# Performance work log

Hardware: AMD Instinct MI355X
Metric: run time of the kernel (lower is better)

The kernel has to match this reference:

```python
import jax, jax.numpy as jnp
import numpy as np

N_NODES, N_EDGES, B, K = 10000, 100000, 8192, 10
MEM = EMB = TE = EF = 172
HID = 80
MSG = 2 * MEM + TE + EF  # 688


def setup_inputs() -> dict:
    key = jax.random.key(0)
    ks = jax.random.split(key, 24)
    f = jax.random.normal
    inp = {
        'timestamps': jax.random.uniform(ks[0], (B,)) * 100.0,
        'edge_features': f(ks[1], (N_EDGES, EF)),
        'temporal_node_features': f(ks[2], (N_NODES, MEM)),
        'node_mem': 0.1 * f(ks[3], (N_NODES, MEM)),
        'last_updated': jax.random.uniform(ks[4], (N_NODES,)) * 50.0,
        'nbr_edge_times': jax.random.uniform(ks[5], (B, K)) * 100.0,
        # TimeEncode params (fixed init from source)
        'time_w': jnp.asarray(1.0 / 10 ** np.linspace(0, 9, TE), jnp.float32),
        'time_b': jnp.zeros((TE,), jnp.float32),
        # RNNCell params
        'rnn_Wih': 0.05 * f(ks[6], (MEM, MSG)),
        'rnn_Whh': 0.05 * f(ks[7], (MEM, MEM)),
        'rnn_bih': jnp.zeros((MEM,)),
        'rnn_bhh': jnp.zeros((MEM,)),
        # layer linears (n_layers=1)
        'lin1_w': 0.05 * f(ks[8], (EMB, EMB + TE + EF)),
        'lin1_b': jnp.zeros((EMB,)),
        'lin2_w': 0.05 * f(ks[9], (EMB, MEM + TE + EMB)),
        'lin2_b': jnp.zeros((EMB,)),
        # MLP head
        'mlp_w1': 0.05 * f(ks[10], (HID, EMB)),
        'mlp_b1': jnp.zeros((HID,)),
        'mlp_w2': 0.05 * f(ks[11], (10, HID)),
        'mlp_b2': jnp.zeros((10,)),
        'mlp_w3': 0.05 * f(ks[12], (1, 10)),
        'mlp_b3': jnp.zeros((1,)),
        'sources': jax.random.randint(ks[13], (B,), 0, N_NODES),
        'destinations': jax.random.randint(ks[14], (B,), 0, N_NODES),
        'edge_idxs': jax.random.randint(ks[15], (B,), 0, N_EDGES),
        'neighbors': jax.random.randint(ks[16], (B, K), 0, N_NODES),
        'nbr_edge_idxs': jax.random.randint(ks[17], (B, K), 0, N_EDGES),
    }
    return inp


def _time_enc(dt, w, b):
    # cos(Linear(1->D)(t)) from TimeEncode
    return jnp.cos(dt[..., None] * w + b)


def reference(timestamps, edge_features, temporal_node_features, node_mem,
              last_updated, nbr_edge_times, time_w, time_b,
              rnn_Wih, rnn_Whh, rnn_bih, rnn_bhh,
              lin1_w, lin1_b, lin2_w, lin2_b,
              mlp_w1, mlp_b1, mlp_w2, mlp_b2, mlp_w3, mlp_b3,
              sources, destinations, edge_idxs, neighbors, nbr_edge_idxs):
    # ---- get_message: gather memories + edge features + time-delta encoding
    ef = edge_features[edge_idxs]                         # [B, EF]
    src_mem = node_mem[sources]                           # [B, MEM]
    dst_mem = node_mem[destinations]                      # [B, MEM]
    dt = timestamps - last_updated[sources]               # [B]
    msg = jnp.concatenate([src_mem, dst_mem, ef, _time_enc(dt, time_w, time_b)], axis=1)  # [B, MSG]

    # ---- message aggregation: keep LAST message per unique source node
    n = node_mem.shape[0]
    b = sources.shape[0]
    last_idx = jnp.full((n,), -1, jnp.int32).at[sources].max(jnp.arange(b, dtype=jnp.int32))
    upd = last_idx >= 0                                   # [N] nodes receiving a message
    gi = jnp.clip(last_idx, 0)
    node_msg = msg[gi]                                    # [N, MSG]

    # ---- RNNCell memory update (masked to updated nodes)
    h_new = jnp.tanh(node_msg @ rnn_Wih.T + rnn_bih + node_mem @ rnn_Whh.T + rnn_bhh)
    mem = jnp.where(upd[:, None], h_new, node_mem)        # [N, MEM]

    # ---- compute_embedding, n_layers = 1 (layer-0 feats = mem + temporal feats)
    src_feat = mem[sources] + temporal_node_features[sources]      # [B, MEM]
    nbr_feat = mem[neighbors] + temporal_node_features[neighbors]  # [B, K, MEM]
    edge_t_enc = _time_enc(timestamps[:, None] - nbr_edge_times, time_w, time_b)  # [B, K, TE]
    nbr_ef = edge_features[nbr_edge_idxs]                           # [B, K, EF]
    nf = jnp.concatenate([nbr_feat, edge_t_enc, nbr_ef], axis=2)    # [B, K, MEM+TE+EF]
    h1 = jnp.einsum('bkf,ef->bke', nf, lin1_w) + lin1_b             # linear_1
    nbr_sum = jax.nn.relu(jnp.sum(h1, axis=1))                      # sum-aggregate, [B, EMB]
    src_t_enc = _time_enc(jnp.zeros_like(timestamps), time_w, time_b)  # cos(b), [B, TE]
    emb = jnp.concatenate([nbr_sum, src_feat, src_t_enc], axis=1) @ lin2_w.T + lin2_b  # [B, EMB]

    # ---- MLP head (dropout disabled / eval mode) + sigmoid
    h = jax.nn.relu(emb @ mlp_w1.T + mlp_b1)
    h = jax.nn.relu(h @ mlp_w2.T + mlp_b2)
    return jax.nn.sigmoid((h @ mlp_w3.T + mlp_b3)[:, 0])  # [B]
```

## Files before the change

### kernel.cpp

```cpp
#include <hip/hip_runtime.h>
#include <math.h>

#define N_NODES 10000
#define BB 8192
#define KK 10
#define D 172
#define HIDD 80

typedef _Float16 f16;
typedef f16 f16x8 __attribute__((ext_vector_type(8)));
typedef f16 f16x4 __attribute__((ext_vector_type(4)));
typedef float f32x4 __attribute__((ext_vector_type(4)));


__global__ void scatter_last(const int* __restrict__ sources, int* __restrict__ last_idx) {
    int b = blockIdx.x * blockDim.x + threadIdx.x;
    if (b < BB) atomicMax(&last_idx[sources[b]], b);
}

__global__ void compact_nodes(const int* __restrict__ last_idx, int* __restrict__ nid,
                              int* __restrict__ li_arr, int* __restrict__ cnt) {
    int n = blockIdx.x * blockDim.x + threadIdx.x;
    if (n < N_NODES) {
        int li = last_idx[n];
        if (li >= 0) { int p = atomicAdd(cnt, 1); nid[p] = n; li_arr[p] = li; }
    }
}

#define CR0 135168
#define CR1 (CR0 + 104448)
#define CR2 (CR1 + 67584)
#define CR3 (CR2 + 15360)
#define CR4 (CR3 + 192)
#define CR5 (CR4 + 220000)
#define CR6 (CR5 + 10001)

__global__ __launch_bounds__(256) void conv_weights(
    const float* __restrict__ Wih, const float* __restrict__ Whh,
    const float* __restrict__ lin1_w, const float* __restrict__ lin2_w,
    const float* __restrict__ w1,
    const float* __restrict__ bih, const float* __restrict__ bhh,
    const float* __restrict__ lin2_b, const float* __restrict__ tb,
    const float* __restrict__ node_mem, const float* __restrict__ tnf,
    f16* __restrict__ Wc, f16* __restrict__ W1, f16* __restrict__ W2,
    f16* __restrict__ Wm1, float* __restrict__ bcomb, float* __restrict__ embc,
    f16* __restrict__ FEAT, int* __restrict__ last_idx, int* __restrict__ cnt)
{
    const int idx = blockIdx.x * 256 + threadIdx.x;
    if (idx < CR0) {
        int n = idx / 704, k = idx % 704, seg = k / 176, kk = k % 176;
        float v = 0.f;
        if (n < D && kk < D) {
            v = Wih[n * 688 + seg * D + kk];
            if (seg == 0) v += Whh[n * D + kk];
        }
        Wc[idx] = (f16)v;
    } else if (idx < CR1) {
        int i = idx - CR0;
        int n = i / 544, k = i % 544, seg = k / 176, kk = k % 176;
        float v = 0.f;
        if (n < D && seg < 3 && kk < D) v = lin1_w[n * 516 + seg * D + kk];
        W1[i] = (f16)v;
    } else if (idx < CR2) {
        int i = idx - CR1;
        int n = i / 352, k = i % 352, seg = k / 176, kk = k % 176;
        float v = 0.f;
        if (n < D && kk < D) v = lin2_w[n * 516 + seg * D + kk];
        W2[i] = (f16)v;
    } else if (idx < CR3) {
        int i = idx - CR2;
        int n = i / 192, k = i % 192;
        Wm1[i] = (f16)((k < D) ? w1[n * D + k] : 0.f);
    } else if (idx < CR4) {
        int i = idx - CR3;
        if (i < D) {
            bcomb[i] = bih[i] + bhh[i];
            float acc = lin2_b[i];
            for (int j = 0; j < D; ++j) acc += lin2_w[i * 516 + 344 + j] * __cosf(tb[j]);
            embc[i] = acc;
        }
    } else if (idx < CR5) {
        int i = idx - CR4;
        int n = i / 22, k0 = (i % 22) * 8;
        f16x8 o;
        #pragma unroll
        for (int j = 0; j < 8; ++j) {
            int kk = k0 + j;
            float v = (kk < D) ? node_mem[(size_t)n * D + kk] + tnf[(size_t)n * D + kk] : 0.f;
            o[j] = (f16)v;
        }
        *(f16x8*)(FEAT + (size_t)n * 176 + k0) = o;
    } else if (idx < CR6) {
        int i = idx - CR5;
        if (i < N_NODES) last_idx[i] = -1;
        else *cnt = 0;
    }
}

#define LDA_R 712

__global__ __launch_bounds__(768) void gemm_rnn_fused(
    const f16* __restrict__ Wc, const float* __restrict__ bcomb,
    const int* __restrict__ nid, const int* __restrict__ li_arr, const int* __restrict__ cnt,
    const int* __restrict__ destinations, const int* __restrict__ edge_idxs,
    const float* __restrict__ timestamps, const float* __restrict__ last_updated,
    const float* __restrict__ node_mem, const float* __restrict__ edge_features,
    const float* __restrict__ tw, const float* __restrict__ tb,
    const float* __restrict__ tnf, f16* __restrict__ FEAT)
{
    const int c = *cnt;
    const int R0 = blockIdx.x * 16;
    if (R0 >= c) return;
    __shared__ f16 As[16 * LDA_R];
    __shared__ int s_n[16], s_dst[16], s_ei[16];
    __shared__ float s_dt[16];
    const int t = threadIdx.x;
    if (t < 16) {
        int i = R0 + t; if (i > c - 1) i = c - 1;
        int n = nid[i], li = li_arr[i];
        s_n[t] = n; s_dst[t] = destinations[li]; s_ei[t] = edge_idxs[li];
        s_dt[t] = timestamps[li] - last_updated[n];
    }
    __syncthreads();
    for (int idx = t; idx < 16 * 88; idx += 768) {
        int row = idx / 88, sub = idx - row * 88;
        int seg = sub / 22, cpos = sub - seg * 22, k0 = cpos * 8;
        f16x8 o;
        if (seg < 3) {
            int n = (seg == 0) ? s_n[row] : (seg == 1) ? s_dst[row] : s_ei[row];
            const float* src = ((seg < 2) ? node_mem : edge_features) + (size_t)n * D + k0;
            float4 lo = *(const float4*)src;
            float4 hi = (cpos < 21) ? *(const float4*)(src + 4) : make_float4(0.f, 0.f, 0.f, 0.f);
            o[0] = (f16)lo.x; o[1] = (f16)lo.y; o[2] = (f16)lo.z; o[3] = (f16)lo.w;
            o[4] = (f16)hi.x; o[5] = (f16)hi.y; o[6] = (f16)hi.z; o[7] = (f16)hi.w;
        } else {
            float dt = s_dt[row];
            #pragma unroll
            for (int j = 0; j < 8; ++j) {
                int kk = k0 + j;
                o[j] = (f16)((kk < D) ? __cosf(dt * tw[kk] + tb[kk]) : 0.f);
            }
        }
        *(f16x8*)(As + row * LDA_R + seg * 176 + k0) = o;
    }
    __syncthreads();
    const int w = t >> 6, l = t & 63;
    if (w >= 11) return;
    const int lane16 = l & 15, koff = (l >> 4) * 8;
    const int C0 = w * 16;
    const f16* Al = As + lane16 * LDA_R + koff;
    const f16* Bp = Wc + (size_t)(C0 + lane16) * 704 + koff;
    f32x4 acc = {};
    #pragma unroll 2
    for (int s = 0; s < 22; ++s) {
        f16x8 a = *(const f16x8*)(Al + s * 32);
        f16x8 b = *(const f16x8*)(Bp + s * 32);
        acc = __builtin_amdgcn_mfma_f32_16x16x32_f16(a, b, acc, 0, 0, 0);
    }
    const int col = C0 + lane16;
    const int rloc = (l >> 4) * 4;
    if (col < D) {
        const float bc = bcomb[col];
        #pragma unroll
        for (int reg = 0; reg < 4; ++reg) {
            int rl = rloc + reg;
            int r = R0 + rl;
            if (r >= c) continue;
            int n = s_n[rl];
            FEAT[(size_t)n * 176 + col] = (f16)(tanhf(acc[reg] + bc) + tnf[(size_t)n * D + col]);
        }
    }
}

#define LDA_1 552
#define LDA_2 360
#define LDE  200

__global__ __launch_bounds__(768) void embed_fused(
    const f16* __restrict__ W1, const float* __restrict__ lin1_b,
    const f16* __restrict__ W2, const float* __restrict__ embc,
    const f16* __restrict__ Wm1, const float* __restrict__ b1,
    const float* __restrict__ w2, const float* __restrict__ b2,
    const float* __restrict__ w3, const float* __restrict__ b3,
    const f16* __restrict__ FEAT, const float* __restrict__ edge_features,
    const float* __restrict__ timestamps, const float* __restrict__ nbr_edge_times,
    const int* __restrict__ neighbors, const int* __restrict__ nbr_edge_idxs,
    const int* __restrict__ sources,
    const float* __restrict__ tw, const float* __restrict__ tb,
    float* __restrict__ out)
{
    __shared__ f16 As[16 * LDA_1];
    __shared__ f16 Acat[16 * LDA_2];
    __shared__ float sH[16][84];
    __shared__ float s_w2[10 * HIDD];
    __shared__ float s_b2[10], s_w3[10], s_b3;
    __shared__ int s_nbr[160], s_nei[160], s_src[16];
    __shared__ float s_net[160], s_ts[16];
    const int t = threadIdx.x;
    const int R0 = blockIdx.x * 16;
    for (int i = t; i < 10 * HIDD; i += 768) s_w2[i] = w2[i];
    if (t < 10) { s_b2[t] = b2[t]; s_w3[t] = w3[t]; }
    if (t == 10) s_b3 = b3[0];
    if (t >= 64 && t < 224) {
        int u = t - 64;
        s_nbr[u] = neighbors[R0 * KK + u];
    } else if (t >= 224 && t < 384) {
        int u = t - 224;
        s_nei[u] = nbr_edge_idxs[R0 * KK + u];
        s_net[u] = nbr_edge_times[R0 * KK + u];
    } else if (t >= 384 && t < 400) {
        s_ts[t - 384] = timestamps[R0 + t - 384];
    } else if (t >= 400 && t < 416) {
        s_src[t - 400] = sources[R0 + t - 400];
    }
    __syncthreads();
    for (int idx = t; idx < 16 * 90 + 16 * 22; idx += 768) {
        if (idx < 16 * 90) {
            int row = idx / 90, c = idx - row * 90;
            if (c < 22) {
                int k0 = c * 8;
                f16x8 v[KK];
                #pragma unroll
                for (int k = 0; k < KK; ++k)
                    v[k] = *(const f16x8*)(FEAT + (size_t)s_nbr[row * KK + k] * 176 + k0);
                float a[8] = {};
                #pragma unroll
                for (int k = 0; k < KK; ++k) {
                    #pragma unroll
                    for (int j = 0; j < 8; ++j) a[j] += (float)v[k][j];
                }
                f16x8 o;
                #pragma unroll
                for (int j = 0; j < 8; ++j) o[j] = (f16)a[j];
                *(f16x8*)(As + row * LDA_1 + k0) = o;
            } else if (c < 44) {
                int k0 = (c - 22) * 8;
                float ts = s_ts[row];
                f16x8 o;
                #pragma unroll
                for (int j = 0; j < 8; ++j) {
                    int kk = k0 + j;
                    float a = 0.f;
                    if (kk < D) {
                        float w = tw[kk], bb = tb[kk];
                        #pragma unroll
                        for (int k = 0; k < KK; ++k) a += __cosf((ts - s_net[row * KK + k]) * w + bb);
                    }
                    o[j] = (f16)a;
                }
                *(f16x8*)(As + row * LDA_1 + 176 + k0) = o;
            } else if (c < 88) {
                int cc = c - 44;
                f16x4 o;
                if (cc == 43) {
                    o[0] = o[1] = o[2] = o[3] = (f16)0.f;
                } else {
                    float4 e[KK];
                    #pragma unroll
                    for (int k = 0; k < KK; ++k)
                        e[k] = *(const float4*)(edge_features + (size_t)s_nei[row * KK + k] * D + cc * 4);
                    float a0 = 0.f, a1 = 0.f, a2 = 0.f, a3 = 0.f;
                    #pragma unroll
                    for (int k = 0; k < KK; ++k) { a0 += e[k].x; a1 += e[k].y; a2 += e[k].z; a3 += e[k].w; }
                    o[0] = (f16)a0; o[1] = (f16)a1; o[2] = (f16)a2; o[3] = (f16)a3;
                }
                *(f16x4*)(As + row * LDA_1 + 352 + cc * 4) = o;
            } else {
                f16x8 z = {};
                *(f16x8*)(As + row * LDA_1 + 528 + (c - 88) * 8) = z;
            }
        } else {
            int j = idx - 16 * 90;
            int row = j / 22, cc = j - row * 22;
            *(f16x8*)(Acat + row * LDA_2 + 176 + cc * 8) =
                *(const f16x8*)(FEAT + (size_t)s_src[row] * 176 + cc * 8);
        }
    }
    __syncthreads();
    const int w = t >> 6, l = t & 63;
    const int lane16 = l & 15, koff = (l >> 4) * 8;
    const int rloc = (l >> 4) * 4;
    const int C0 = w * 16;
    if (w < 11) {
        const f16* Al = As + lane16 * LDA_1 + koff;
        const f16* Bp = W1 + (size_t)(C0 + lane16) * 544 + koff;
        f32x4 acc = {};
        #pragma unroll 2
        for (int s = 0; s < 17; ++s) {
            f16x8 a = *(const f16x8*)(Al + s * 32);
            f16x8 b = *(const f16x8*)(Bp + s * 32);
            acc = __builtin_amdgcn_mfma_f32_16x16x32_f16(a, b, acc, 0, 0, 0);
        }
        const int col = C0 + lane16;
        if (col < 176) {
            const float bb = (col < D) ? 10.0f * lin1_b[col] : 0.f;
            #pragma unroll
            for (int reg = 0; reg < 4; ++reg) {
                int r = rloc + reg;
                Acat[r * LDA_2 + col] = (col < D) ? (f16)fmaxf(acc[reg] + bb, 0.f) : (f16)0.f;
            }
        }
    }
    __syncthreads();
    f16* Emb = As;
    if (w < 11) {
        const f16* Al = Acat + lane16 * LDA_2 + koff;
        const f16* Bp = W2 + (size_t)(C0 + lane16) * 352 + koff;
        f32x4 acc = {};
        #pragma unroll 2
        for (int s = 0; s < 11; ++s) {
            f16x8 a = *(const f16x8*)(Al + s * 32);
            f16x8 b = *(const f16x8*)(Bp + s * 32);
            acc = __builtin_amdgcn_mfma_f32_16x16x32_f16(a, b, acc, 0, 0, 0);
        }
        const int col = C0 + lane16;
        const float ec = (col < D) ? embc[col] : 0.f;
        #pragma unroll
        for (int reg = 0; reg < 4; ++reg) {
            int r = rloc + reg;
            Emb[r * LDE + col] = (col < D) ? (f16)(acc[reg] + ec) : (f16)0.f;
        }
    }
    __syncthreads();
    if (w < 5) {
        const int Cm = w * 16;
        const f16* Bp = Wm1 + (size_t)(Cm + lane16) * 192 + koff;
        const f16* Al = Emb + (lane16) * LDE + koff;
        f32x4 acc = {};
        #pragma unroll
        for (int s = 0; s < 6; ++s) {
            f16x8 a = *(const f16x8*)(Al + s * 32);
            f16x8 b = *(const f16x8*)(Bp + s * 32);
            acc = __builtin_amdgcn_mfma_f32_16x16x32_f16(a, b, acc, 0, 0, 0);
        }
        const int col = Cm + lane16;
        #pragma unroll
        for (int reg = 0; reg < 4; ++reg)
            sH[rloc + reg][col] = fmaxf(acc[reg] + b1[col], 0.f);
    }
    __syncthreads();
    if (t < 16) {
        float h2[10];
        #pragma unroll
        for (int j = 0; j < 10; ++j) h2[j] = s_b2[j];
        for (int f = 0; f < HIDD; ++f) {
            float hv = sH[t][f];
            #pragma unroll
            for (int j = 0; j < 10; ++j) h2[j] = fmaf(hv, s_w2[j * HIDD + f], h2[j]);
        }
        float logit = s_b3;
        #pragma unroll
        for (int j = 0; j < 10; ++j) logit += fmaxf(h2[j], 0.f) * s_w3[j];
        out[R0 + t] = 1.f / (1.f + expf(-logit));
    }
}


extern "C" void kernel_launch(void* const* d_in, const int* in_sizes, int n_in,
                              void* d_out, int out_size, void* d_ws, size_t ws_size,
                              hipStream_t stream) {
    const float* timestamps     = (const float*)d_in[0];
    const float* edge_features  = (const float*)d_in[1];
    const float* tnf            = (const float*)d_in[2];
    const float* node_mem       = (const float*)d_in[3];
    const float* last_updated   = (const float*)d_in[4];
    const float* nbr_edge_times = (const float*)d_in[5];
    const float* time_w         = (const float*)d_in[6];
    const float* time_b         = (const float*)d_in[7];
    const float* Wih            = (const float*)d_in[8];
    const float* Whh            = (const float*)d_in[9];
    const float* bih            = (const float*)d_in[10];
    const float* bhh            = (const float*)d_in[11];
    const float* lin1_w         = (const float*)d_in[12];
    const float* lin1_b         = (const float*)d_in[13];
    const float* lin2_w         = (const float*)d_in[14];
    const float* lin2_b         = (const float*)d_in[15];
    const float* w1             = (const float*)d_in[16];
    const float* b1             = (const float*)d_in[17];
    const float* w2             = (const float*)d_in[18];
    const float* b2             = (const float*)d_in[19];
    const float* w3             = (const float*)d_in[20];
    const float* b3             = (const float*)d_in[21];
    const int* sources          = (const int*)d_in[22];
    const int* destinations     = (const int*)d_in[23];
    const int* edge_idxs        = (const int*)d_in[24];
    const int* neighbors        = (const int*)d_in[25];
    const int* nbr_edge_idxs    = (const int*)d_in[26];
    float* out = (float*)d_out;

    char* p = (char*)d_ws;
    auto bump = [&p](size_t bytes) { char* r = p; p += (bytes + 255) & ~(size_t)255; return r; };
    int* last_idx = (int*)bump(N_NODES * 4);
    int* nid      = (int*)bump(N_NODES * 4);
    int* li_arr   = (int*)bump(N_NODES * 4);
    int* cnt      = (int*)bump(256);
    f16* Wc16     = (f16*)bump((size_t)192 * 704 * 2);
    f16* W1_16    = (f16*)bump((size_t)192 * 544 * 2);
    f16* W2_16    = (f16*)bump((size_t)192 * 352 * 2);
    f16* Wm1_16   = (f16*)bump((size_t)80 * 192 * 2);
    float* bcomb  = (float*)bump(D * 4);
    float* embc   = (float*)bump(D * 4);
    f16* FEAT16   = (f16*)bump((size_t)N_NODES * 176 * 2);

    hipLaunchKernelGGL(conv_weights, dim3((CR6 + 255) / 256), dim3(256), 0, stream,
                       Wih, Whh, lin1_w, lin2_w, w1, bih, bhh, lin2_b, time_b,
                       node_mem, tnf, Wc16, W1_16, W2_16, Wm1_16, bcomb, embc,
                       FEAT16, last_idx, cnt);

    hipLaunchKernelGGL(scatter_last, dim3(BB / 256), dim3(256), 0, stream, sources, last_idx);
    hipLaunchKernelGGL(compact_nodes, dim3((N_NODES + 255) / 256), dim3(256), 0, stream,
                       last_idx, nid, li_arr, cnt);

    hipLaunchKernelGGL(gemm_rnn_fused, dim3((N_NODES + 15) / 16), dim3(768), 0, stream,
                       Wc16, bcomb, nid, li_arr, cnt, destinations, edge_idxs,
                       timestamps, last_updated, node_mem, edge_features,
                       time_w, time_b, tnf, FEAT16);

    hipLaunchKernelGGL(embed_fused, dim3(BB / 16), dim3(768), 0, stream,
                       W1_16, lin1_b, W2_16, embc, Wm1_16, b1, w2, b2, w3, b3,
                       FEAT16, edge_features, timestamps, nbr_edge_times,
                       neighbors, nbr_edge_idxs, sources, time_w, time_b, out);
}
```

Before: 90.54 us.

## Fuse all stages into one persistent cooperative kernel with grid syncs

Replaces the five separate launches (weight conversion, scatter, compaction, RNN GEMM, embedding) with one cooperative kernel of 256 persistent blocks. Stages are separated by grid-wide syncs, and the GEMM stages loop over tiles. Shared memory is a union of the two stage layouts. This removes launch gaps and the per-launch overheads. In exchange it limits parallelism to 256 blocks of 768 threads and adds grid barrier costs, so tile-level occupancy and latency hiding may drop.

```diff
diff --git a/kernel.cpp b/kernel.cpp
--- a/kernel.cpp
+++ b/kernel.cpp
@@ -1,5 +1,8 @@
 #include <hip/hip_runtime.h>
+#include <hip/hip_cooperative_groups.h>
 #include <math.h>
+
+namespace cg = cooperative_groups;
 
 #define N_NODES 10000
 #define BB 8192
@@ -11,21 +14,6 @@
 typedef f16 f16x8 __attribute__((ext_vector_type(8)));
 typedef f16 f16x4 __attribute__((ext_vector_type(4)));
 typedef float f32x4 __attribute__((ext_vector_type(4)));
-
-
-__global__ void scatter_last(const int* __restrict__ sources, int* __restrict__ last_idx) {
-    int b = blockIdx.x * blockDim.x + threadIdx.x;
-    if (b < BB) atomicMax(&last_idx[sources[b]], b);
-}
-
-__global__ void compact_nodes(const int* __restrict__ last_idx, int* __restrict__ nid,
-                              int* __restrict__ li_arr, int* __restrict__ cnt) {
-    int n = blockIdx.x * blockDim.x + threadIdx.x;
-    if (n < N_NODES) {
-        int li = last_idx[n];
-        if (li >= 0) { int p = atomicAdd(cnt, 1); nid[p] = n; li_arr[p] = li; }
-    }
-}
 
 #define CR0 135168
 #define CR1 (CR0 + 104448)
@@ -35,323 +23,338 @@
 #define CR5 (CR4 + 220000)
 #define CR6 (CR5 + 10001)
 
-__global__ __launch_bounds__(256) void conv_weights(
+#define LDA_R 712
+#define LDA_1 552
+#define LDA_2 360
+#define LDE  200
+
+struct RnnS {
+    f16 As[16 * LDA_R];
+    int s_n[16], s_dst[16], s_ei[16];
+    float s_dt[16];
+};
+struct EmbS {
+    f16 As[16 * LDA_1];
+    f16 Acat[16 * LDA_2];
+    float sH[16][84];
+    float s_w2[10 * HIDD];
+    float s_b2[10], s_w3[10], s_b3;
+    int s_nbr[160], s_nei[160], s_src[16];
+    float s_net[160], s_ts[16];
+};
+#define SMEM_BYTES (sizeof(EmbS) > sizeof(RnnS) ? sizeof(EmbS) : sizeof(RnnS))
+
+__global__ __launch_bounds__(768) void tgn_mega(
+    const float* __restrict__ timestamps, const float* __restrict__ edge_features,
+    const float* __restrict__ tnf, const float* __restrict__ node_mem,
+    const float* __restrict__ last_updated, const float* __restrict__ nbr_edge_times,
+    const float* __restrict__ tw, const float* __restrict__ tb,
     const float* __restrict__ Wih, const float* __restrict__ Whh,
-    const float* __restrict__ lin1_w, const float* __restrict__ lin2_w,
-    const float* __restrict__ w1,
     const float* __restrict__ bih, const float* __restrict__ bhh,
-    const float* __restrict__ lin2_b, const float* __restrict__ tb,
-    const float* __restrict__ node_mem, const float* __restrict__ tnf,
-    f16* __restrict__ Wc, f16* __restrict__ W1, f16* __restrict__ W2,
-    f16* __restrict__ Wm1, float* __restrict__ bcomb, float* __restrict__ embc,
-    f16* __restrict__ FEAT, int* __restrict__ last_idx, int* __restrict__ cnt)
+    const float* __restrict__ lin1_w, const float* __restrict__ lin1_b,
+    const float* __restrict__ lin2_w, const float* __restrict__ lin2_b,
+    const float* __restrict__ w1, const float* __restrict__ b1,
+    const float* __restrict__ w2, const float* __restrict__ b2,
+    const float* __restrict__ w3, const float* __restrict__ b3,
+    const int* __restrict__ sources, const int* __restrict__ destinations,
+    const int* __restrict__ edge_idxs, const int* __restrict__ neighbors,
+    const int* __restrict__ nbr_edge_idxs,
+    f16* Wc, f16* W1, f16* W2, f16* Wm1,
+    float* bcomb, float* embc, f16* FEAT,
+    int* last_idx, int* nid, int* li_arr, int* cnt, float* out)
 {
-    const int idx = blockIdx.x * 256 + threadIdx.x;
-    if (idx < CR0) {
-        int n = idx / 704, k = idx % 704, seg = k / 176, kk = k % 176;
-        float v = 0.f;
-        if (n < D && kk < D) {
-            v = Wih[n * 688 + seg * D + kk];
-            if (seg == 0) v += Whh[n * D + kk];
-        }
-        Wc[idx] = (f16)v;
-    } else if (idx < CR1) {
-        int i = idx - CR0;
-        int n = i / 544, k = i % 544, seg = k / 176, kk = k % 176;
-        float v = 0.f;
-        if (n < D && seg < 3 && kk < D) v = lin1_w[n * 516 + seg * D + kk];
-        W1[i] = (f16)v;
-    } else if (idx < CR2) {
-        int i = idx - CR1;
-        int n = i / 352, k = i % 352, seg = k / 176, kk = k % 176;
-        float v = 0.f;
-        if (n < D && kk < D) v = lin2_w[n * 516 + seg * D + kk];
-        W2[i] = (f16)v;
-    } else if (idx < CR3) {
-        int i = idx - CR2;
-        int n = i / 192, k = i % 192;
-        Wm1[i] = (f16)((k < D) ? w1[n * D + k] : 0.f);
-    } else if (idx < CR4) {
-        int i = idx - CR3;
-        if (i < D) {
-            bcomb[i] = bih[i] + bhh[i];
-            float acc = lin2_b[i];
-            for (int j = 0; j < D; ++j) acc += lin2_w[i * 516 + 344 + j] * __cosf(tb[j]);
-            embc[i] = acc;
-        }
-    } else if (idx < CR5) {
-        int i = idx - CR4;
-        int n = i / 22, k0 = (i % 22) * 8;
-        f16x8 o;
-        #pragma unroll
-        for (int j = 0; j < 8; ++j) {
-            int kk = k0 + j;
-            float v = (kk < D) ? node_mem[(size_t)n * D + kk] + tnf[(size_t)n * D + kk] : 0.f;
-            o[j] = (f16)v;
-        }
-        *(f16x8*)(FEAT + (size_t)n * 176 + k0) = o;
-    } else if (idx < CR6) {
-        int i = idx - CR5;
-        if (i < N_NODES) last_idx[i] = -1;
-        else *cnt = 0;
-    }
-}
-
-#define LDA_R 712
-
-__global__ __launch_bounds__(768) void gemm_rnn_fused(
-    const f16* __restrict__ Wc, const float* __restrict__ bcomb,
-    const int* __restrict__ nid, const int* __restrict__ li_arr, const int* __restrict__ cnt,
-    const int* __restrict__ destinations, const int* __restrict__ edge_idxs,
-    const float* __restrict__ timestamps, const float* __restrict__ last_updated,
-    const float* __restrict__ node_mem, const float* __restrict__ edge_features,
-    const float* __restrict__ tw, const float* __restrict__ tb,
-    const float* __restrict__ tnf, f16* __restrict__ FEAT)
-{
-    const int c = *cnt;
-    const int R0 = blockIdx.x * 16;
-    if (R0 >= c) return;
-    __shared__ f16 As[16 * LDA_R];
-    __shared__ int s_n[16], s_dst[16], s_ei[16];
-    __shared__ float s_dt[16];
+    __shared__ __align__(16) char smem[SMEM_BYTES];
     const int t = threadIdx.x;
-    if (t < 16) {
-        int i = R0 + t; if (i > c - 1) i = c - 1;
-        int n = nid[i], li = li_arr[i];
-        s_n[t] = n; s_dst[t] = destinations[li]; s_ei[t] = edge_idxs[li];
-        s_dt[t] = timestamps[li] - last_updated[n];
-    }
-    __syncthreads();
-    for (int idx = t; idx < 16 * 88; idx += 768) {
-        int row = idx / 88, sub = idx - row * 88;
-        int seg = sub / 22, cpos = sub - seg * 22, k0 = cpos * 8;
-        f16x8 o;
-        if (seg < 3) {
-            int n = (seg == 0) ? s_n[row] : (seg == 1) ? s_dst[row] : s_ei[row];
-            const float* src = ((seg < 2) ? node_mem : edge_features) + (size_t)n * D + k0;
-            float4 lo = *(const float4*)src;
-            float4 hi = (cpos < 21) ? *(const float4*)(src + 4) : make_float4(0.f, 0.f, 0.f, 0.f);
-            o[0] = (f16)lo.x; o[1] = (f16)lo.y; o[2] = (f16)lo.z; o[3] = (f16)lo.w;
-            o[4] = (f16)hi.x; o[5] = (f16)hi.y; o[6] = (f16)hi.z; o[7] = (f16)hi.w;
-        } else {
-            float dt = s_dt[row];
+    cg::grid_group grid = cg::this_grid();
+
+    for (int idx = blockIdx.x * 768 + t; idx < CR6; idx += 256 * 768) {
+        if (idx < CR0) {
+            int n = idx / 704, k = idx % 704, seg = k / 176, kk = k % 176;
+            float v = 0.f;
+            if (n < D && kk < D) {
+                v = Wih[n * 688 + seg * D + kk];
+                if (seg == 0) v += Whh[n * D + kk];
+            }
+            Wc[idx] = (f16)v;
+        } else if (idx < CR1) {
+            int i = idx - CR0;
+            int n = i / 544, k = i % 544, seg = k / 176, kk = k % 176;
+            float v = 0.f;
+            if (n < D && seg < 3 && kk < D) v = lin1_w[n * 516 + seg * D + kk];
+            W1[i] = (f16)v;
+        } else if (idx < CR2) {
+            int i = idx - CR1;
+            int n = i / 352, k = i % 352, seg = k / 176, kk = k % 176;
+            float v = 0.f;
+            if (n < D && kk < D) v = lin2_w[n * 516 + seg * D + kk];
+            W2[i] = (f16)v;
+        } else if (idx < CR3) {
+            int i = idx - CR2;
+            int n = i / 192, k = i % 192;
+            Wm1[i] = (f16)((k < D) ? w1[n * D + k] : 0.f);
+        } else if (idx < CR4) {
+            int i = idx - CR3;
+            if (i < D) {
+                bcomb[i] = bih[i] + bhh[i];
+                float acc = lin2_b[i];
+                for (int j = 0; j < D; ++j) acc += lin2_w[i * 516 + 344 + j] * __cosf(tb[j]);
+                embc[i] = acc;
+            }
+        } else if (idx < CR5) {
+            int i = idx - CR4;
+            int n = i / 22, k0 = (i % 22) * 8;
+            f16x8 o;
             #pragma unroll
             for (int j = 0; j < 8; ++j) {
                 int kk = k0 + j;
-                o[j] = (f16)((kk < D) ? __cosf(dt * tw[kk] + tb[kk]) : 0.f);
-            }
-        }
-        *(f16x8*)(As + row * LDA_R + seg * 176 + k0) = o;
-    }
-    __syncthreads();
-    const int w = t >> 6, l = t & 63;
-    if (w >= 11) return;
-    const int lane16 = l & 15, koff = (l >> 4) * 8;
-    const int C0 = w * 16;
-    const f16* Al = As + lane16 * LDA_R + koff;
-    const f16* Bp = Wc + (size_t)(C0 + lane16) * 704 + koff;
-    f32x4 acc = {};
-    #pragma unroll 2
-    for (int s = 0; s < 22; ++s) {
-        f16x8 a = *(const f16x8*)(Al + s * 32);
-        f16x8 b = *(const f16x8*)(Bp + s * 32);
-        acc = __builtin_amdgcn_mfma_f32_16x16x32_f16(a, b, acc, 0, 0, 0);
-    }
-    const int col = C0 + lane16;
-    const int rloc = (l >> 4) * 4;
-    if (col < D) {
-        const float bc = bcomb[col];
-        #pragma unroll
-        for (int reg = 0; reg < 4; ++reg) {
-            int rl = rloc + reg;
-            int r = R0 + rl;
-            if (r >= c) continue;
-            int n = s_n[rl];
-            FEAT[(size_t)n * 176 + col] = (f16)(tanhf(acc[reg] + bc) + tnf[(size_t)n * D + col]);
+                float v = (kk < D) ? node_mem[(size_t)n * D + kk] + tnf[(size_t)n * D + kk] : 0.f;
+                o[j] = (f16)v;
+            }
+            *(f16x8*)(FEAT + (size_t)n * 176 + k0) = o;
+        } else {
+            int i = idx - CR5;
+            if (i < N_NODES) last_idx[i] = -1;
+            else *cnt = 0;
         }
     }
-}
-
-#define LDA_1 552
-#define LDA_2 360
-#define LDE  200
-
-__global__ __launch_bounds__(768) void embed_fused(
-    const f16* __restrict__ W1, const float* __restrict__ lin1_b,
-    const f16* __restrict__ W2, const float* __restrict__ embc,
-    const f16* __restrict__ Wm1, const float* __restrict__ b1,
-    const float* __restrict__ w2, const float* __restrict__ b2,
-    const float* __restrict__ w3, const float* __restrict__ b3,
-    const f16* __restrict__ FEAT, const float* __restrict__ edge_features,
-    const float* __restrict__ timestamps, const float* __restrict__ nbr_edge_times,
-    const int* __restrict__ neighbors, const int* __restrict__ nbr_edge_idxs,
-    const int* __restrict__ sources,
-    const float* __restrict__ tw, const float* __restrict__ tb,
-    float* __restrict__ out)
-{
-    __shared__ f16 As[16 * LDA_1];
-    __shared__ f16 Acat[16 * LDA_2];
-    __shared__ float sH[16][84];
-    __shared__ float s_w2[10 * HIDD];
-    __shared__ float s_b2[10], s_w3[10], s_b3;
-    __shared__ int s_nbr[160], s_nei[160], s_src[16];
-    __shared__ float s_net[160], s_ts[16];
-    const int t = threadIdx.x;
-    const int R0 = blockIdx.x * 16;
-    for (int i = t; i < 10 * HIDD; i += 768) s_w2[i] = w2[i];
-    if (t < 10) { s_b2[t] = b2[t]; s_w3[t] = w3[t]; }
-    if (t == 10) s_b3 = b3[0];
-    if (t >= 64 && t < 224) {
-        int u = t - 64;
-        s_nbr[u] = neighbors[R0 * KK + u];
-    } else if (t >= 224 && t < 384) {
-        int u = t - 224;
-        s_nei[u] = nbr_edge_idxs[R0 * KK + u];
-        s_net[u] = nbr_edge_times[R0 * KK + u];
-    } else if (t >= 384 && t < 400) {
-        s_ts[t - 384] = timestamps[R0 + t - 384];
-    } else if (t >= 400 && t < 416) {
-        s_src[t - 400] = sources[R0 + t - 400];
+    grid.sync();
+
+    for (int b = blockIdx.x * 768 + t; b < BB; b += 256 * 768)
+        atomicMax(&last_idx[sources[b]], b);
+    grid.sync();
+
+    for (int n = blockIdx.x * 768 + t; n < N_NODES; n += 256 * 768) {
+        int li = last_idx[n];
+        if (li >= 0) { int p = atomicAdd(cnt, 1); nid[p] = n; li_arr[p] = li; }
     }
-    __syncthreads();
-    for (int idx = t; idx < 16 * 90 + 16 * 22; idx += 768) {
-        if (idx < 16 * 90) {
-            int row = idx / 90, c = idx - row * 90;
-            if (c < 22) {
-                int k0 = c * 8;
-                f16x8 v[KK];
-                #pragma unroll
-                for (int k = 0; k < KK; ++k)
-                    v[k] = *(const f16x8*)(FEAT + (size_t)s_nbr[row * KK + k] * 176 + k0);
-                float a[8] = {};
-                #pragma unroll
-                for (int k = 0; k < KK; ++k) {
+    grid.sync();
+
+    const int wv = t >> 6, l = t & 63;
+    const int lane16 = l & 15, koff = (l >> 4) * 8;
+    const int rloc = (l >> 4) * 4;
+
+    {
+        const int c = *(volatile int*)cnt;
+        const int ntiles = (c + 15) >> 4;
+        RnnS& rs = *reinterpret_cast<RnnS*>(smem);
+        for (int tile = blockIdx.x; tile < ntiles; tile += 256) {
+            const int R0 = tile * 16;
+            __syncthreads();
+            if (t < 16) {
+                int i = R0 + t; if (i > c - 1) i = c - 1;
+                int n = nid[i], li = li_arr[i];
+                rs.s_n[t] = n; rs.s_dst[t] = destinations[li]; rs.s_ei[t] = edge_idxs[li];
+                rs.s_dt[t] = timestamps[li] - last_updated[n];
+            }
+            __syncthreads();
+            for (int idx = t; idx < 16 * 88; idx += 768) {
+                int row = idx / 88, sub = idx - row * 88;
+                int seg = sub / 22, cpos = sub - seg * 22, k0 = cpos * 8;
+                f16x8 o;
+                if (seg < 3) {
+                    int n = (seg == 0) ? rs.s_n[row] : (seg == 1) ? rs.s_dst[row] : rs.s_ei[row];
+                    const float* src = ((seg < 2) ? node_mem : edge_features) + (size_t)n * D + k0;
+                    float4 lo = *(const float4*)src;
+                    float4 hi = (cpos < 21) ? *(const float4*)(src + 4) : make_float4(0.f, 0.f, 0.f, 0.f);
+                    o[0] = (f16)lo.x; o[1] = (f16)lo.y; o[2] = (f16)lo.z; o[3] = (f16)lo.w;
+                    o[4] = (f16)hi.x; o[5] = (f16)hi.y; o[6] = (f16)hi.z; o[7] = (f16)hi.w;
+                } else {
+                    float dt = rs.s_dt[row];
                     #pragma unroll
-                    for (int j = 0; j < 8; ++j) a[j] += (float)v[k][j];
-                }
-                f16x8 o;
-                #pragma unroll
-                for (int j = 0; j < 8; ++j) o[j] = (f16)a[j];
-                *(f16x8*)(As + row * LDA_1 + k0) = o;
-            } else if (c < 44) {
-                int k0 = (c - 22) * 8;
-                float ts = s_ts[row];
-                f16x8 o;
-                #pragma unroll
-                for (int j = 0; j < 8; ++j) {
-                    int kk = k0 + j;
-                    float a = 0.f;
-                    if (kk < D) {
-                        float w = tw[kk], bb = tb[kk];
-                        #pragma unroll
-                        for (int k = 0; k < KK; ++k) a += __cosf((ts - s_net[row * KK + k]) * w + bb);
+                    for (int j = 0; j < 8; ++j) {
+                        int kk = k0 + j;
+                        o[j] = (f16)((kk < D) ? __cosf(dt * tw[kk] + tb[kk]) : 0.f);
                     }
-                    o[j] = (f16)a;
-                }
-                *(f16x8*)(As + row * LDA_1 + 176 + k0) = o;
-            } else if (c < 88) {
-                int cc = c - 44;
-                f16x4 o;
-                if (cc == 43) {
-                    o[0] = o[1] = o[2] = o[3] = (f16)0.f;
-                } else {
-                    float4 e[KK];
+                }
+                *(f16x8*)(rs.As + row * LDA_R + seg * 176 + k0) = o;
+            }
+            __syncthreads();
+            if (wv < 11) {
+                const int C0 = wv * 16;
+                const f16* Al = rs.As + lane16 * LDA_R + koff;
+                const f16* Bp = Wc + (size_t)(C0 + lane16) * 704 + koff;
+                f32x4 acc = {};
+                #pragma unroll 2
+                for (int s = 0; s < 22; ++s) {
+                    f16x8 a = *(const f16x8*)(Al + s * 32);
+                    f16x8 b = *(const f16x8*)(Bp + s * 32);
+                    acc = __builtin_amdgcn_mfma_f32_16x16x32_f16(a, b, acc, 0, 0, 0);
+                }
+                const int col = C0 + lane16;
+                if (col < D) {
+                    const float bc = bcomb[col];
                     #pragma unroll
-                    for (int k = 0; k < KK; ++k)
-                        e[k] = *(const float4*)(edge_features + (size_t)s_nei[row * KK + k] * D + cc * 4);
-                    float a0 = 0.f, a1 = 0.f, a2 = 0.f, a3 = 0.f;
-                    #pragma unroll
-                    for (int k = 0; k < KK; ++k) { a0 += e[k].x; a1 += e[k].y; a2 += e[k].z; a3 += e[k].w; }
-                    o[0] = (f16)a0; o[1] = (f16)a1; o[2] = (f16)a2; o[3] = (f16)a3;
-                }
-                *(f16x4*)(As + row * LDA_1 + 352 + cc * 4) = o;
-            } else {
-                f16x8 z = {};
-                *(f16x8*)(As + row * LDA_1 + 528 + (c - 88) * 8) = z;
-            }
-        } else {
-            int j = idx - 16 * 90;
-            int row = j / 22, cc = j - row * 22;
-            *(f16x8*)(Acat + row * LDA_2 + 176 + cc * 8) =
-                *(const f16x8*)(FEAT + (size_t)s_src[row] * 176 + cc * 8);
+                    for (int reg = 0; reg < 4; ++reg) {
+                        int rl = rloc + reg;
+                        int r = R0 + rl;
+                        if (r >= c) continue;
+                        int n = rs.s_n[rl];
+                        FEAT[(size_t)n * 176 + col] = (f16)(tanhf(acc[reg] + bc) + tnf[(size_t)n * D + col]);
+                    }
+                }
+            }
         }
     }
-    __syncthreads();
-    const int w = t >> 6, l = t & 63;
-    const int lane16 = l & 15, koff = (l >> 4) * 8;
-    const int rloc = (l >> 4) * 4;
-    const int C0 = w * 16;
-    if (w < 11) {
-        const f16* Al = As + lane16 * LDA_1 + koff;
-        const f16* Bp = W1 + (size_t)(C0 + lane16) * 544 + koff;
-        f32x4 acc = {};
-        #pragma unroll 2
-        for (int s = 0; s < 17; ++s) {
-            f16x8 a = *(const f16x8*)(Al + s * 32);
-            f16x8 b = *(const f16x8*)(Bp + s * 32);
-            acc = __builtin_amdgcn_mfma_f32_16x16x32_f16(a, b, acc, 0, 0, 0);
+    grid.sync();
+
+    {
+        EmbS& es = *reinterpret_cast<EmbS*>(smem);
+        for (int i = t; i < 10 * HIDD; i += 768) es.s_w2[i] = w2[i];
+        if (t < 10) { es.s_b2[t] = b2[t]; es.s_w3[t] = w3[t]; }
+        if (t == 10) es.s_b3 = b3[0];
+        for (int tile = blockIdx.x; tile < BB / 16; tile += 256) {
+            const int R0 = tile * 16;
+            __syncthreads();
+            if (t >= 64 && t < 224) {
+                int u = t - 64;
+                es.s_nbr[u] = neighbors[R0 * KK + u];
+            } else if (t >= 224 && t < 384) {
+                int u = t - 224;
+                es.s_nei[u] = nbr_edge_idxs[R0 * KK + u];
+                es.s_net[u] = nbr_edge_times[R0 * KK + u];
+            } else if (t >= 384 && t < 400) {
+                es.s_ts[t - 384] = timestamps[R0 + t - 384];
+            } else if (t >= 400 && t < 416) {
+                es.s_src[t - 400] = sources[R0 + t - 400];
+            }
+            __syncthreads();
+            for (int idx = t; idx < 16 * 90 + 16 * 22; idx += 768) {
+                if (idx < 16 * 90) {
+                    int row = idx / 90, c = idx - row * 90;
+                    if (c < 22) {
+                        int k0 = c * 8;
+                        f16x8 v[KK];
+                        #pragma unroll
+                        for (int k = 0; k < KK; ++k)
+                            v[k] = *(const f16x8*)(FEAT + (size_t)es.s_nbr[row * KK + k] * 176 + k0);
+                        float a[8] = {};
+                        #pragma unroll
+                        for (int k = 0; k < KK; ++k) {
+                            #pragma unroll
+                            for (int j = 0; j < 8; ++j) a[j] += (float)v[k][j];
+                        }
+                        f16x8 o;
+                        #pragma unroll
+                        for (int j = 0; j < 8; ++j) o[j] = (f16)a[j];
+                        *(f16x8*)(es.As + row * LDA_1 + k0) = o;
+                    } else if (c < 44) {
+                        int k0 = (c - 22) * 8;
+                        float ts = es.s_ts[row];
+                        f16x8 o;
+                        #pragma unroll
+                        for (int j = 0; j < 8; ++j) {
+                            int kk = k0 + j;
+                            float a = 0.f;
+                            if (kk < D) {
+                                float w = tw[kk], bb2 = tb[kk];
+                                #pragma unroll
+                                for (int k = 0; k < KK; ++k) a += __cosf((ts - es.s_net[row * KK + k]) * w + bb2);
+                            }
+                            o[j] = (f16)a;
+                        }
+                        *(f16x8*)(es.As + row * LDA_1 + 176 + k0) = o;
+                    } else if (c < 88) {
+                        int cc = c - 44;
+                        f16x4 o;
+                        if (cc == 43) {
+                            o[0] = o[1] = o[2] = o[3] = (f16)0.f;
+                        } else {
+                            float4 e[KK];
+                            #pragma unroll
+                            for (int k = 0; k < KK; ++k)
+                                e[k] = *(const float4*)(edge_features + (size_t)es.s_nei[row * KK + k] * D + cc * 4);
+                            float a0 = 0.f, a1 = 0.f, a2 = 0.f, a3 = 0.f;
+                            #pragma unroll
+                            for (int k = 0; k < KK; ++k) { a0 += e[k].x; a1 += e[k].y; a2 += e[k].z; a3 += e[k].w; }
+                            o[0] = (f16)a0; o[1] = (f16)a1; o[2] = (f16)a2; o[3] = (f16)a3;
+                        }
+                        *(f16x4*)(es.As + row * LDA_1 + 352 + cc * 4) = o;
+                    } else {
+                        f16x8 z = {};
+                        *(f16x8*)(es.As + row * LDA_1 + 528 + (c - 88) * 8) = z;
+                    }
+                } else {
+                    int j = idx - 16 * 90;
+                    int row = j / 22, cc = j - row * 22;
+                    *(f16x8*)(es.Acat + row * LDA_2 + 176 + cc * 8) =
+                        *(const f16x8*)(FEAT + (size_t)es.s_src[row] * 176 + cc * 8);
+                }
+            }
+            __syncthreads();
+            const int C0 = wv * 16;
+            if (wv < 11) {
+                const f16* Al = es.As + lane16 * LDA_1 + koff;
+                const f16* Bp = W1 + (size_t)(C0 + lane16) * 544 + koff;
+                f32x4 acc = {};
+                #pragma unroll 2
+                for (int s = 0; s < 17; ++s) {
+                    f16x8 a = *(const f16x8*)(Al + s * 32);
+                    f16x8 b = *(const f16x8*)(Bp + s * 32);
+                    acc = __builtin_amdgcn_mfma_f32_16x16x32_f16(a, b, acc, 0, 0, 0);
+                }
+                const int col = C0 + lane16;
+                if (col < 176) {
+                    const float bb2 = (col < D) ? 10.0f * lin1_b[col] : 0.f;
+                    #pragma unroll
+                    for (int reg = 0; reg < 4; ++reg) {
+                        int r = rloc + reg;
+                        es.Acat[r * LDA_2 + col] = (col < D) ? (f16)fmaxf(acc[reg] + bb2, 0.f) : (f16)0.f;
+                    }
+                }
+            }
+            __syncthreads();
+            f16* Emb = es.As;
+            if (wv < 11) {
+                const f16* Al = es.Acat + lane16 * LDA_2 + koff;
+                const f16* Bp = W2 + (size_t)(C0 + lane16) * 352 + koff;
+                f32x4 acc = {};
+                #pragma unroll 2
+                for (int s = 0; s < 11; ++s) {
+                    f16x8 a = *(const f16x8*)(Al + s * 32);
+                    f16x8 b = *(const f16x8*)(Bp + s * 32);
+                    acc = __builtin_amdgcn_mfma_f32_16x16x32_f16(a, b, acc, 0, 0, 0);
+                }
+                const int col = C0 + lane16;
+                const float ec = (col < D) ? embc[col] : 0.f;
+                #pragma unroll
+                for (int reg = 0; reg < 4; ++reg) {
+                    int r = rloc + reg;
+                    Emb[r * LDE + col] = (col < D) ? (f16)(acc[reg] + ec) : (f16)0.f;
+                }
+            }
+            __syncthreads();
+            if (wv < 5) {
+                const int Cm = wv * 16;
+                const f16* Bp = Wm1 + (size_t)(Cm + lane16) * 192 + koff;
+                const f16* Al = Emb + lane16 * LDE + koff;
+                f32x4 acc = {};
+                #pragma unroll
+                for (int s = 0; s < 6; ++s) {
+                    f16x8 a = *(const f16x8*)(Al + s * 32);
+                    f16x8 b = *(const f16x8*)(Bp + s * 32);
+                    acc = __builtin_amdgcn_mfma_f32_16x16x32_f16(a, b, acc, 0, 0, 0);
+                }
+                const int col = Cm + lane16;
+                #pragma unroll
+                for (int reg = 0; reg < 4; ++reg)
+                    es.sH[rloc + reg][col] = fmaxf(acc[reg] + b1[col], 0.f);
+            }
+            __syncthreads();
+            if (t < 16) {
+                float h2[10];
+                #pragma unroll
+                for (int j = 0; j < 10; ++j) h2[j] = es.s_b2[j];
+                for (int f = 0; f < HIDD; ++f) {
+                    float hv = es.sH[t][f];
+                    #pragma unroll
+                    for (int j = 0; j < 10; ++j) h2[j] = fmaf(hv, es.s_w2[j * HIDD + f], h2[j]);
+                }
+                float logit = es.s_b3;
+                #pragma unroll
+                for (int j = 0; j < 10; ++j) logit += fmaxf(h2[j], 0.f) * es.s_w3[j];
+                out[R0 + t] = 1.f / (1.f + expf(-logit));
+            }
         }
-        const int col = C0 + lane16;
-        if (col < 176) {
-            const float bb = (col < D) ? 10.0f * lin1_b[col] : 0.f;
-            #pragma unroll
-            for (int reg = 0; reg < 4; ++reg) {
-                int r = rloc + reg;
-                Acat[r * LDA_2 + col] = (col < D) ? (f16)fmaxf(acc[reg] + bb, 0.f) : (f16)0.f;
-            }
-        }
-    }
-    __syncthreads();
-    f16* Emb = As;
-    if (w < 11) {
-        const f16* Al = Acat + lane16 * LDA_2 + koff;
-        const f16* Bp = W2 + (size_t)(C0 + lane16) * 352 + koff;
-        f32x4 acc = {};
-        #pragma unroll 2
-        for (int s = 0; s < 11; ++s) {
-            f16x8 a = *(const f16x8*)(Al + s * 32);
-            f16x8 b = *(const f16x8*)(Bp + s * 32);
-            acc = __builtin_amdgcn_mfma_f32_16x16x32_f16(a, b, acc, 0, 0, 0);
-        }
-        const int col = C0 + lane16;
-        const float ec = (col < D) ? embc[col] : 0.f;
-        #pragma unroll
-        for (int reg = 0; reg < 4; ++reg) {
-            int r = rloc + reg;
-            Emb[r * LDE + col] = (col < D) ? (f16)(acc[reg] + ec) : (f16)0.f;
-        }
-    }
-    __syncthreads();
-    if (w < 5) {
-        const int Cm = w * 16;
-        const f16* Bp = Wm1 + (size_t)(Cm + lane16) * 192 + koff;
-        const f16* Al = Emb + (lane16) * LDE + koff;
-        f32x4 acc = {};
-        #pragma unroll
-        for (int s = 0; s < 6; ++s) {
-            f16x8 a = *(const f16x8*)(Al + s * 32);
-            f16x8 b = *(const f16x8*)(Bp + s * 32);
-            acc = __builtin_amdgcn_mfma_f32_16x16x32_f16(a, b, acc, 0, 0, 0);
-        }
-        const int col = Cm + lane16;
-        #pragma unroll
-        for (int reg = 0; reg < 4; ++reg)
-            sH[rloc + reg][col] = fmaxf(acc[reg] + b1[col], 0.f);
-    }
-    __syncthreads();
-    if (t < 16) {
-        float h2[10];
-        #pragma unroll
-        for (int j = 0; j < 10; ++j) h2[j] = s_b2[j];
-        for (int f = 0; f < HIDD; ++f) {
-            float hv = sH[t][f];
-            #pragma unroll
-            for (int j = 0; j < 10; ++j) h2[j] = fmaf(hv, s_w2[j * HIDD + f], h2[j]);
-        }
-        float logit = s_b3;
-        #pragma unroll
-        for (int j = 0; j < 10; ++j) logit += fmaxf(h2[j], 0.f) * s_w3[j];
-        out[R0 + t] = 1.f / (1.f + expf(-logit));
     }
 }
 
@@ -402,22 +405,17 @@
     float* embc   = (float*)bump(D * 4);
     f16* FEAT16   = (f16*)bump((size_t)N_NODES * 176 * 2);
 
-    hipLaunchKernelGGL(conv_weights, dim3((CR6 + 255) / 256), dim3(256), 0, stream,
-                       Wih, Whh, lin1_w, lin2_w, w1, bih, bhh, lin2_b, time_b,
-                       node_mem, tnf, Wc16, W1_16, W2_16, Wm1_16, bcomb, embc,
-                       FEAT16, last_idx, cnt);
-
-    hipLaunchKernelGGL(scatter_last, dim3(BB / 256), dim3(256), 0, stream, sources, last_idx);
-    hipLaunchKernelGGL(compact_nodes, dim3((N_NODES + 255) / 256), dim3(256), 0, stream,
-                       last_idx, nid, li_arr, cnt);
-
-    hipLaunchKernelGGL(gemm_rnn_fused, dim3((N_NODES + 15) / 16), dim3(768), 0, stream,
-                       Wc16, bcomb, nid, li_arr, cnt, destinations, edge_idxs,
-                       timestamps, last_updated, node_mem, edge_features,
-                       time_w, time_b, tnf, FEAT16);
-
-    hipLaunchKernelGGL(embed_fused, dim3(BB / 16), dim3(768), 0, stream,
-                       W1_16, lin1_b, W2_16, embc, Wm1_16, b1, w2, b2, w3, b3,
-                       FEAT16, edge_features, timestamps, nbr_edge_times,
-                       neighbors, nbr_edge_idxs, sources, time_w, time_b, out);
+    void* args[] = {
+        (void*)&timestamps, (void*)&edge_features, (void*)&tnf, (void*)&node_mem,
+        (void*)&last_updated, (void*)&nbr_edge_times, (void*)&time_w, (void*)&time_b,
+        (void*)&Wih, (void*)&Whh, (void*)&bih, (void*)&bhh,
+        (void*)&lin1_w, (void*)&lin1_b, (void*)&lin2_w, (void*)&lin2_b,
+        (void*)&w1, (void*)&b1, (void*)&w2, (void*)&b2, (void*)&w3, (void*)&b3,
+        (void*)&sources, (void*)&destinations, (void*)&edge_idxs, (void*)&neighbors,
+        (void*)&nbr_edge_idxs,
+        (void*)&Wc16, (void*)&W1_16, (void*)&W2_16, (void*)&Wm1_16,
+        (void*)&bcomb, (void*)&embc, (void*)&FEAT16,
+        (void*)&last_idx, (void*)&nid, (void*)&li_arr, (void*)&cnt, (void*)&out
+    };
+    hipLaunchCooperativeKernel((const void*)tgn_mega, dim3(256), dim3(768), args, 0, stream);
 }
```

New measurement: 227.7 us. +151.5%, slower.

## Drop node compaction kernel; run RNN GEMM over all nodes directly by index

Applied to the files above, without the earlier changes.

Removes the compact_nodes kernel and its atomic counter, so the RNN GEMM kernel walks every node in fixed 16-row tiles and uses last_idx to decide which rows to write back. This saves one kernel launch and the atomic-append pass, and makes node order deterministic. The cost is that all 625 blocks now gather and multiply, including rows for nodes that were never updated, where before only about 5.6k compacted rows were processed. Non-updated rows are masked out on store.

```diff
diff --git a/kernel.cpp b/kernel.cpp
--- a/kernel.cpp
+++ b/kernel.cpp
@@ -16,15 +16,6 @@
 __global__ void scatter_last(const int* __restrict__ sources, int* __restrict__ last_idx) {
     int b = blockIdx.x * blockDim.x + threadIdx.x;
     if (b < BB) atomicMax(&last_idx[sources[b]], b);
-}
-
-__global__ void compact_nodes(const int* __restrict__ last_idx, int* __restrict__ nid,
-                              int* __restrict__ li_arr, int* __restrict__ cnt) {
-    int n = blockIdx.x * blockDim.x + threadIdx.x;
-    if (n < N_NODES) {
-        int li = last_idx[n];
-        if (li >= 0) { int p = atomicAdd(cnt, 1); nid[p] = n; li_arr[p] = li; }
-    }
 }
 
 #define CR0 135168
@@ -33,7 +24,7 @@
 #define CR3 (CR2 + 15360)
 #define CR4 (CR3 + 192)
 #define CR5 (CR4 + 220000)
-#define CR6 (CR5 + 10001)
+#define CR6 (CR5 + 10000)
 
 __global__ __launch_bounds__(256) void conv_weights(
     const float* __restrict__ Wih, const float* __restrict__ Whh,
@@ -44,7 +35,7 @@
     const float* __restrict__ node_mem, const float* __restrict__ tnf,
     f16* __restrict__ Wc, f16* __restrict__ W1, f16* __restrict__ W2,
     f16* __restrict__ Wm1, float* __restrict__ bcomb, float* __restrict__ embc,
-    f16* __restrict__ FEAT, int* __restrict__ last_idx, int* __restrict__ cnt)
+    f16* __restrict__ FEAT, int* __restrict__ last_idx)
 {
     const int idx = blockIdx.x * 256 + threadIdx.x;
     if (idx < CR0) {
@@ -91,9 +82,7 @@
         }
         *(f16x8*)(FEAT + (size_t)n * 176 + k0) = o;
     } else if (idx < CR6) {
-        int i = idx - CR5;
-        if (i < N_NODES) last_idx[i] = -1;
-        else *cnt = 0;
+        last_idx[idx - CR5] = -1;
     }
 }
 
@@ -101,25 +90,26 @@
 
 __global__ __launch_bounds__(768) void gemm_rnn_fused(
     const f16* __restrict__ Wc, const float* __restrict__ bcomb,
-    const int* __restrict__ nid, const int* __restrict__ li_arr, const int* __restrict__ cnt,
+    const int* __restrict__ last_idx,
     const int* __restrict__ destinations, const int* __restrict__ edge_idxs,
     const float* __restrict__ timestamps, const float* __restrict__ last_updated,
     const float* __restrict__ node_mem, const float* __restrict__ edge_features,
     const float* __restrict__ tw, const float* __restrict__ tb,
     const float* __restrict__ tnf, f16* __restrict__ FEAT)
 {
-    const int c = *cnt;
     const int R0 = blockIdx.x * 16;
-    if (R0 >= c) return;
     __shared__ f16 As[16 * LDA_R];
-    __shared__ int s_n[16], s_dst[16], s_ei[16];
+    __shared__ int s_li[16], s_dst[16], s_ei[16];
     __shared__ float s_dt[16];
     const int t = threadIdx.x;
     if (t < 16) {
-        int i = R0 + t; if (i > c - 1) i = c - 1;
-        int n = nid[i], li = li_arr[i];
-        s_n[t] = n; s_dst[t] = destinations[li]; s_ei[t] = edge_idxs[li];
-        s_dt[t] = timestamps[li] - last_updated[n];
+        int n = R0 + t;
+        int li = last_idx[n];
+        int lic = li < 0 ? 0 : li;
+        s_li[t] = li;
+        s_dst[t] = destinations[lic];
+        s_ei[t]  = edge_idxs[lic];
+        s_dt[t]  = (li < 0) ? 0.f : timestamps[li] - last_updated[n];
     }
     __syncthreads();
     for (int idx = t; idx < 16 * 88; idx += 768) {
@@ -127,7 +117,7 @@
         int seg = sub / 22, cpos = sub - seg * 22, k0 = cpos * 8;
         f16x8 o;
         if (seg < 3) {
-            int n = (seg == 0) ? s_n[row] : (seg == 1) ? s_dst[row] : s_ei[row];
+            int n = (seg == 0) ? (R0 + row) : (seg == 1) ? s_dst[row] : s_ei[row];
             const float* src = ((seg < 2) ? node_mem : edge_features) + (size_t)n * D + k0;
             float4 lo = *(const float4*)src;
             float4 hi = (cpos < 21) ? *(const float4*)(src + 4) : make_float4(0.f, 0.f, 0.f, 0.f);
@@ -164,9 +154,8 @@
         #pragma unroll
         for (int reg = 0; reg < 4; ++reg) {
             int rl = rloc + reg;
-            int r = R0 + rl;
-            if (r >= c) continue;
-            int n = s_n[rl];
+            if (s_li[rl] < 0) continue;
+            int n = R0 + rl;
             FEAT[(size_t)n * 176 + col] = (f16)(tanhf(acc[reg] + bc) + tnf[(size_t)n * D + col]);
         }
     }
@@ -391,9 +380,6 @@
     char* p = (char*)d_ws;
     auto bump = [&p](size_t bytes) { char* r = p; p += (bytes + 255) & ~(size_t)255; return r; };
     int* last_idx = (int*)bump(N_NODES * 4);
-    int* nid      = (int*)bump(N_NODES * 4);
-    int* li_arr   = (int*)bump(N_NODES * 4);
-    int* cnt      = (int*)bump(256);
     f16* Wc16     = (f16*)bump((size_t)192 * 704 * 2);
     f16* W1_16    = (f16*)bump((size_t)192 * 544 * 2);
     f16* W2_16    = (f16*)bump((size_t)192 * 352 * 2);
@@ -405,14 +391,12 @@
     hipLaunchKernelGGL(conv_weights, dim3((CR6 + 255) / 256), dim3(256), 0, stream,
                        Wih, Whh, lin1_w, lin2_w, w1, bih, bhh, lin2_b, time_b,
                        node_mem, tnf, Wc16, W1_16, W2_16, Wm1_16, bcomb, embc,
-                       FEAT16, last_idx, cnt);
+                       FEAT16, last_idx);
 
     hipLaunchKernelGGL(scatter_last, dim3(BB / 256), dim3(256), 0, stream, sources, last_idx);
-    hipLaunchKernelGGL(compact_nodes, dim3((N_NODES + 255) / 256), dim3(256), 0, stream,
-                       last_idx, nid, li_arr, cnt);
-
-    hipLaunchKernelGGL(gemm_rnn_fused, dim3((N_NODES + 15) / 16), dim3(768), 0, stream,
-                       Wc16, bcomb, nid, li_arr, cnt, destinations, edge_idxs,
+
+    hipLaunchKernelGGL(gemm_rnn_fused, dim3(N_NODES / 16), dim3(768), 0, stream,
+                       Wc16, bcomb, last_idx, destinations, edge_idxs,
                        timestamps, last_updated, node_mem, edge_features,
                        time_w, time_b, tnf, FEAT16);
 
```

Result: slower. 108.3 us (+19.6%).
